# Kernel optimization log

Measured on AMD Instinct MI355X. Metric: run time of the kernel, lower is better.

Reference implementation:

```python
import jax, jax.numpy as jnp
import numpy as np

H = 16        # num heads
ALPHA = 1.3   # entmax alpha
N_ITER = 50   # bisection iterations
EPS = 1e-5    # layernorm eps


def entmax_bisect(x, alpha=ALPHA, n_iter=N_ITER):
    # x: (..., K). Bisection entmax along last axis (Peters et al. 2019).
    am1 = alpha - 1.0
    x = x - jnp.max(x, axis=-1, keepdims=True)
    m = jnp.max(x, axis=-1, keepdims=True)  # == 0 after shift
    lo, hi = m - 10.0, m + 10.0
    def step(carry, _):
        lo, hi = carry
        mid = 0.5 * (lo + hi)
        p = jnp.maximum(am1 * x - mid, 0.0) ** (1.0 / am1)
        gt = jnp.sum(p, axis=-1, keepdims=True) > 1.0
        return (jnp.where(gt, mid, lo), jnp.where(gt, hi, mid)), None
    (lo, hi), _ = jax.lax.scan(jax.checkpoint(step), (lo, hi), None, length=n_iter)
    p = jnp.maximum(am1 * x - hi, 0.0) ** (1.0 / am1)
    return p / (jnp.sum(p, axis=-1, keepdims=True) + 1e-12)


def _heads(t, B, N, hd):
    return t.reshape(B, N, H, hd).transpose(0, 2, 1, 3)  # (B,H,N,hd)


def attn_branch(x, mask, wq, bq, wk, bk, wv, bv, wo, bo, use_entmax):
    B, N, D = x.shape
    hd = D // H
    q = _heads(x @ wq + bq, B, N, hd)
    k = _heads(x @ wk + bk, B, N, hd)
    v = _heads(x @ wv + bv, B, N, hd)
    s = jnp.einsum('bhqd,bhkd->bhqk', q, k) / float(np.sqrt(hd)) + mask
    if use_entmax:
        s = s - jnp.max(s, axis=-1, keepdims=True)
        a = entmax_bisect(s)
    else:
        a = jax.nn.softmax(s, axis=-1)
    o = jnp.einsum('bhqk,bhkd->bhqd', a, v).transpose(0, 2, 1, 3).reshape(B, N, D)
    return o @ wo + bo


def layer_norm(x, g, b):
    m = jnp.mean(x, axis=-1, keepdims=True)
    v = jnp.mean((x - m) ** 2, axis=-1, keepdims=True)
    return (x - m) * jax.lax.rsqrt(v + EPS) * g + b


def setup_inputs():
    B, N, D, F, FILM, NMODS = 4, 512, 2048, 8192, 64, 10000
    key = jax.random.key(0)
    ks = iter(jax.random.split(key, 64))
    rn = lambda *s: jax.random.normal(next(ks), s, dtype=jnp.float32)
    inp = dict(
        x=rn(B, N, D),
        attn_mask_intra=jnp.zeros((N, N), jnp.float32),
        attn_mask_inter=jnp.zeros((N, N), jnp.float32),
        mods=jax.random.randint(next(ks), (B, N), 0, 9999),
        film_emb=rn(NMODS, FILM) * 0.02,
        film_gw=rn(FILM, D) * 0.02, film_gb=jnp.zeros((D,), jnp.float32),
        film_bw=rn(FILM, D) * 0.02, film_bb=jnp.zeros((D,), jnp.float32),
        gate_alpha=jnp.zeros((2,), jnp.float32),
        ln1_g=jnp.ones((D,), jnp.float32), ln1_b=jnp.zeros((D,), jnp.float32),
        ln2_g=jnp.ones((D,), jnp.float32), ln2_b=jnp.zeros((D,), jnp.float32),
        ffn_w1=rn(D, F) * 0.02, ffn_b1=jnp.zeros((F,), jnp.float32),
        ffn_w2=rn(F, D) * 0.02, ffn_b2=jnp.zeros((D,), jnp.float32),
    )
    for tag in ('a', 'e'):
        for nm in ('q', 'k', 'v', 'o'):
            inp['w%s_%s' % (nm, tag)] = rn(D, D) * 0.02
            inp['b%s_%s' % (nm, tag)] = jnp.zeros((D,), jnp.float32)
    return inp


def reference(x, attn_mask_intra, attn_mask_inter, mods,
              film_emb, film_gw, film_gb, film_bw, film_bb,
              gate_alpha, ln1_g, ln1_b, ln2_g, ln2_b,
              ffn_w1, ffn_b1, ffn_w2, ffn_b2,
              wq_a, bq_a, wk_a, bk_a, wv_a, bv_a, wo_a, bo_a,
              wq_e, bq_e, wk_e, bk_e, wv_e, bv_e, wo_e, bo_e):
    # FiLM modulation on the intra-module branch input
    e = film_emb[jnp.clip(mods, 1, None)]                      # (B,N,FILM)
    y_intra = (1.0 + e @ film_gw + film_gb) * x + (e @ film_bw + film_bb)
    z_intra = attn_branch(y_intra, attn_mask_intra, wq_a, bq_a, wk_a, bk_a,
                          wv_a, bv_a, wo_a, bo_a, use_entmax=False)
    z_inter = attn_branch(x, attn_mask_inter, wq_e, bq_e, wk_e, bk_e,
                          wv_e, bv_e, wo_e, bo_e, use_entmax=True)
    w = jax.nn.softmax(gate_alpha)                              # global gate
    z = w[0] * z_intra + w[1] * z_inter
    h = layer_norm(x + z, ln1_g, ln1_b)                         # Post-LN
    y = jax.nn.relu(h @ ffn_w1 + ffn_b1) @ ffn_w2 + ffn_b2
    return layer_norm(h + y, ln2_g, ln2_b)
```

## Files before the change

### kernel.cpp

```cpp
#include <hip/hip_runtime.h>
#include <hip/hip_bf16.h>

typedef float f32x4 __attribute__((ext_vector_type(4)));
typedef short bf16x8 __attribute__((ext_vector_type(8)));
typedef unsigned short u16;

#define SEQ    512
#define DIM    2048
#define NHEAD  16
#define HDIM   128
#define BATCH  4
#define BTOK   2048
#define FFDIM  8192
#define DSZ    ((long)BTOK*DIM)
#define QKVN   (3*DIM)
#define QKVSZ  ((long)BTOK*QKVN)
#define ISS    0.08838834764831845f

__device__ __forceinline__ u16 f2bf(float f){
  union{float fv;unsigned u;}c;c.fv=f;
  unsigned r=c.u+0x7FFFu+((c.u>>16)&1u); return (u16)(r>>16);
}
__device__ __forceinline__ float bf2f(u16 v){
  union{unsigned u;float f;}c;c.u=((unsigned)v)<<16;return c.f;
}
__device__ __forceinline__ float pow103(float t){
  return __builtin_amdgcn_exp2f(__builtin_amdgcn_logf(t)*(10.0f/3.0f));
}

#define GLD16(g,l) __builtin_amdgcn_global_load_lds( \
    (const __attribute__((address_space(1))) unsigned int*)(g), \
    (__attribute__((address_space(3))) unsigned int*)(l), 16, 0, 0)

#define MF(a,b,c) __builtin_amdgcn_mfma_f32_16x16x32_bf16(a,b,c,0,0,0)
#define VMW(n) do{ asm volatile("s_waitcnt vmcnt(" #n ")" ::: "memory"); \
                   __builtin_amdgcn_sched_barrier(0); }while(0)
#define LGKM0() do{ asm volatile("s_waitcnt lgkmcnt(0)" ::: "memory"); \
                    __builtin_amdgcn_sched_barrier(0); }while(0)
#define BARR() do{ asm volatile("" ::: "memory"); __builtin_amdgcn_s_barrier(); \
                   asm volatile("" ::: "memory"); }while(0)

__global__ __launch_bounds__(256, 2)
void gemm4w(const u16* __restrict__ A, int lda, long sAo, long sAi,
            const u16* __restrict__ B, int ldb, long sBo, long sBi,
            u16* __restrict__ C, int ldc, long sCo,
            const float* __restrict__ bias, long sbias,
            int K, int hdiv, int relu)
{
  __shared__ __align__(16) u16 sm[36864];
  char* smb = (char*)sm;

  int gx = gridDim.x, gy = gridDim.y;
  int nwg = gx*gy*gridDim.z;
  int flat = (blockIdx.z*gy + blockIdx.y)*gx + blockIdx.x;
  int cpx = nwg >> 3; flat = (flat & 7)*cpx + (flat >> 3);
  int by = flat % gy; int tq = flat / gy; int bx = tq % gx; int bz = tq / gx;

  int zo = bz / hdiv, zi = bz - zo*hdiv;
  const u16* Ab = A + (long)zo*sAo + (long)zi*sAi;
  const u16* Bb = B + (long)zo*sBo + (long)zi*sBi;
  int m0 = by*128, n0 = bx*256;

  int tid = threadIdx.x, lane = tid & 63, w = tid >> 6;
  int lr = lane & 15, lg = lane >> 4;
  int rl = lane >> 2, cbyte = (lane & 3)*16;

  int sRA[2], sCA[2];
  #pragma unroll
  for (int q = 0; q < 2; q++) {
    int r = (2*w+q)*16 + rl;
    sRA[q] = r ^ ((r>>2)&1);
    sCA[q] = (cbyte ^ ((((r>>2)^r)&1)<<4) ^ (((r>>1)&1)<<5)) >> 1;
  }
  int sRB[4], sCB[4];
  #pragma unroll
  for (int q = 0; q < 4; q++) {
    int r = (4*w+q)*16 + rl;
    sRB[q] = r ^ ((r>>2)&1);
    sCB[q] = (cbyte ^ ((((r>>2)^r)&1)<<4) ^ (((r>>1)&1)<<5)) >> 1;
  }

  int aoff = (lr*64 + lg*16) ^ ((lane&7)<<4);
  int boff = w*4096 + ((lr*64 + lg*16) ^ ((lane&7)<<4));

  f32x4 acc[8][4] = {};
  int NT = K >> 5;

  auto STG = [&](int buf, int kt) {
    int kcol = kt*32;
    char* base = smb + buf*24576;
    #pragma unroll
    for (int q = 0; q < 2; q++)
      GLD16(Ab + (long)(m0 + sRA[q])*lda + kcol + sCA[q], base + (2*w+q)*1024);
    #pragma unroll
    for (int q = 0; q < 4; q++)
      GLD16(Bb + (long)(n0 + sRB[q])*ldb + kcol + sCB[q], base + 8192 + (4*w+q)*1024);
  };

  STG(0,0);
  if (NT > 1) STG(1,1);

  int buf = 0;
  for (int t = 0; t < NT; t++) {
    char* Ax = smb + buf*24576;
    char* Bx = Ax + 8192;

    if (t+2 < NT) {
      int nb = buf + 2; if (nb >= 3) nb -= 3;
      STG(nb, t+2);
      VMW(12);
    } else if (t+1 < NT) { VMW(6); }
    else                 { VMW(0); }
    BARR();

    bf16x8 af[8], bv[4];
    #pragma unroll
    for (int i = 0; i < 8; i++) af[i] = *(const bf16x8*)(Ax + aoff + i*1024);
    #pragma unroll
    for (int j = 0; j < 4; j++) bv[j] = *(const bf16x8*)(Bx + boff + j*1024);
    LGKM0();
    __builtin_amdgcn_s_setprio(1);
    #pragma unroll
    for (int i = 0; i < 8; i++) {
      acc[i][0] = MF(af[i], bv[0], acc[i][0]);
      acc[i][1] = MF(af[i], bv[1], acc[i][1]);
      acc[i][2] = MF(af[i], bv[2], acc[i][2]);
      acc[i][3] = MF(af[i], bv[3], acc[i][3]);
    }
    __builtin_amdgcn_s_setprio(0);
    BARR();
    buf++; if (buf == 3) buf = 0;
  }

  u16* Cb = C + (long)bz*sCo;
  #pragma unroll
  for (int j = 0; j < 4; j++) {
    int col = n0 + w*64 + j*16 + lr;
    float bv2 = bias ? bias[zo*sbias + col] : 0.0f;
    #pragma unroll
    for (int i = 0; i < 8; i++) {
      #pragma unroll
      for (int e = 0; e < 4; e++) {
        int row = m0 + i*16 + lg*4 + e;
        float v = acc[i][j][e] + bv2;
        if (relu) v = fmaxf(v, 0.0f);
        Cb[(long)row*ldc + col] = f2bf(v);
      }
    }
  }
}

__global__ __launch_bounds__(256, 3)
void gemm4(const u16* __restrict__ A, int lda, long sAo, long sAi,
           const u16* __restrict__ B, int ldb, long sBo, long sBi,
           void* __restrict__ C, int ldc, long sCo, int outbf,
           const float* __restrict__ bias, long sbias,
           int K, int hdiv, int relu)
{
  __shared__ __align__(16) u16 sm[24576];
  char* smb = (char*)sm;

  int gx = gridDim.x, gy = gridDim.y;
  int nwg = gx*gy*gridDim.z;
  int flat = (blockIdx.z*gy + blockIdx.y)*gx + blockIdx.x;
  int cpx = nwg >> 3; flat = (flat & 7)*cpx + (flat >> 3);
  int by = flat % gy; int tq = flat / gy; int bx = tq % gx; int bz = tq / gx;

  int zo = bz / hdiv, zi = bz - zo*hdiv;
  const u16* Ab = A + (long)zo*sAo + (long)zi*sAi;
  const u16* Bb = B + (long)zo*sBo + (long)zi*sBi;
  int m0 = by*128, n0 = bx*128;

  int tid = threadIdx.x, lane = tid & 63, w = tid >> 6;
  int wrow = (w>>1)*64, wn = (w&1)*64;
  int lr = lane & 15, lg = lane >> 4;

  int stR[2], stC[2], ldsch[2];
  #pragma unroll
  for (int q = 0; q < 2; q++) {
    int chunk = q*4 + w;
    int r = chunk*16 + (lane>>2);
    int c = (lane&3)*16;
    int Rz = r ^ ((r>>2)&1);
    int Cz = c ^ ((((r>>2)^r)&1)<<4) ^ (((r>>1)&1)<<5);
    stR[q] = Rz; stC[q] = Cz>>1;
    ldsch[q] = chunk*1024;
  }

  int aoff = ((wrow + lr)*64 + lg*16) ^ ((lane&7)<<4);
  int boff = ((wn  + lr)*64 + lg*16) ^ ((lane&7)<<4);

  f32x4 acc[4][4] = {};
  int NT = K >> 5;

  auto STG = [&](int buf, int op, int kt) {
    const u16* gp = op ? Bb : Ab;
    int ld   = op ? ldb : lda;
    int base = op ? n0 : m0;
    int kcol = kt*32;
    #pragma unroll
    for (int q = 0; q < 2; q++) {
      const u16* src = gp + (long)(base + stR[q])*ld + kcol + stC[q];
      char* dst = smb + buf*16384 + op*8192 + ldsch[q];
      GLD16(src, dst);
    }
  };

  STG(0,0,0); STG(0,1,0);
  STG(1,0,1); STG(1,1,1);

  int buf = 0;
  for (int t = 0; t < NT; t++) {
    char* Ax = smb + buf*16384;
    char* Bx = smb + buf*16384 + 8192;

    if (t+2 < NT) {
      int nb = buf + 2; if (nb >= 3) nb -= 3;
      STG(nb,0,t+2); STG(nb,1,t+2);
      VMW(8);
    } else if (t+1 < NT) { VMW(4); }
    else                 { VMW(0); }
    BARR();

    bf16x8 af[4], bv[4];
    #pragma unroll
    for (int i = 0; i < 4; i++) af[i] = *(const bf16x8*)(Ax + aoff + i*1024);
    #pragma unroll
    for (int j = 0; j < 4; j++) bv[j] = *(const bf16x8*)(Bx + boff + j*1024);
    LGKM0();
    __builtin_amdgcn_s_setprio(1);
    #pragma unroll
    for (int i = 0; i < 4; i++) {
      acc[i][0] = MF(af[i], bv[0], acc[i][0]);
      acc[i][1] = MF(af[i], bv[1], acc[i][1]);
      acc[i][2] = MF(af[i], bv[2], acc[i][2]);
      acc[i][3] = MF(af[i], bv[3], acc[i][3]);
    }
    __builtin_amdgcn_s_setprio(0);
    BARR();
    buf++; if (buf == 3) buf = 0;
  }

  if (outbf) {
    u16* Cb = (u16*)C + (long)bz*sCo;
    #pragma unroll
    for (int j = 0; j < 4; j++) {
      int col = n0 + wn + j*16 + lr;
      float bv2 = bias ? bias[zo*sbias + col] : 0.0f;
      #pragma unroll
      for (int i = 0; i < 4; i++) {
        #pragma unroll
        for (int e = 0; e < 4; e++) {
          int row = m0 + wrow + i*16 + lg*4 + e;
          float v = acc[i][j][e] + bv2;
          if (relu) v = fmaxf(v, 0.0f);
          Cb[(long)row*ldc + col] = f2bf(v);
        }
      }
    }
  } else {
    float* Cb = (float*)C + (long)bz*sCo;
    #pragma unroll
    for (int j = 0; j < 4; j++) {
      int col = n0 + wn + j*16 + lr;
      #pragma unroll
      for (int i = 0; i < 4; i++) {
        #pragma unroll
        for (int e = 0; e < 4; e++) {
          int row = m0 + wrow + i*16 + lg*4 + e;
          Cb[(long)row*ldc + col] = acc[i][j][e];
        }
      }
    }
  }
}

template<int ENTMAX>
__global__ __launch_bounds__(256, 2)
void qkprobs(const u16* __restrict__ QKVp, long brOff,
             const float* __restrict__ maskp, u16* __restrict__ P)
{
  __shared__ __align__(16) u16 sm[40960];
  char* smb = (char*)sm;

  int m0 = blockIdx.x*64;
  int z  = blockIdx.y;
  int b  = z >> 4, h = z & 15;
  const u16* Qb = QKVp + brOff + (long)b*SEQ*QKVN + h*HDIM;
  const u16* Kb = Qb + DIM;

  int tid = threadIdx.x, lane = tid & 63, w = tid >> 6;
  int lr = lane & 15, lg = lane >> 4;
  int wn = w*128;

  int rl = lane >> 2;
  int cb = (lane & 3)*16;

  int aoff = (lr*64 + lg*16) ^ ((lane&7)<<4);
  int boff = ((wn + lr)*64 + lg*16) ^ ((lane&7)<<4);

  auto stgA = [&](int kt) {
    int r = w*16 + rl;
    int Rz = r ^ ((r>>2)&1);
    int Cz = cb ^ ((((r>>2)^r)&1)<<4) ^ (((r>>1)&1)<<5);
    GLD16(Qb + (long)(m0+Rz)*QKVN + kt*32 + (Cz>>1), smb + kt*4096 + w*1024);
  };
  auto stgB = [&](int buf, int kt) {
    #pragma unroll
    for (int q = 0; q < 8; q++) {
      int chunk = q*4 + w;
      int r = chunk*16 + rl;
      int Rz = r ^ ((r>>2)&1);
      int Cz = cb ^ ((((r>>2)^r)&1)<<4) ^ (((r>>1)&1)<<5);
      GLD16(Kb + (long)Rz*QKVN + kt*32 + (Cz>>1),
            smb + 16384 + buf*32768 + chunk*1024);
    }
  };

  f32x4 acc[4][8] = {};

  stgA(0); stgA(1); stgA(2); stgA(3);
  stgB(0,0);

  #pragma unroll
  for (int kt = 0; kt < 4; kt++) {
    if (kt < 3) { stgB((kt+1)&1, kt+1); VMW(8); } else { VMW(0); }
    BARR();
    char* Bx = smb + 16384 + (kt&1)*32768;
    bf16x8 af[4], bv[8];
    #pragma unroll
    for (int i = 0; i < 4; i++) af[i] = *(const bf16x8*)(smb + kt*4096 + aoff + i*1024);
    #pragma unroll
    for (int j = 0; j < 8; j++) bv[j] = *(const bf16x8*)(Bx + boff + j*1024);
    LGKM0();
    __builtin_amdgcn_s_setprio(1);
    #pragma unroll
    for (int i = 0; i < 4; i++)
      #pragma unroll
      for (int j = 0; j < 8; j++)
        acc[i][j] = MF(af[i], bv[j], acc[i][j]);
    __builtin_amdgcn_s_setprio(0);
    BARR();
  }

  float* redA = (float*)smb;
  float* redB = (float*)(smb + 1024);

  float rmax[16];
  #pragma unroll
  for (int s = 0; s < 16; s++) rmax[s] = -3.4e38f;
  #pragma unroll
  for (int i = 0; i < 4; i++) {
    #pragma unroll
    for (int e = 0; e < 4; e++) {
      int row = i*16 + lg*4 + e;
      const float* mp = maskp + (long)(m0+row)*SEQ + wn + lr;
      #pragma unroll
      for (int j = 0; j < 8; j++) {
        float v = acc[i][j][e]*ISS + mp[j*16];
        acc[i][j][e] = v;
        rmax[i*4+e] = fmaxf(rmax[i*4+e], v);
      }
    }
  }
  #pragma unroll
  for (int s = 0; s < 16; s++)
    #pragma unroll
    for (int o = 1; o < 16; o <<= 1) rmax[s] = fmaxf(rmax[s], __shfl_xor(rmax[s], o));
  if (lr == 0) {
    #pragma unroll
    for (int i = 0; i < 4; i++)
      #pragma unroll
      for (int e = 0; e < 4; e++) redA[w*64 + i*16 + lg*4 + e] = rmax[i*4+e];
  }
  BARR();
  #pragma unroll
  for (int i = 0; i < 4; i++)
    #pragma unroll
    for (int e = 0; e < 4; e++) {
      int row = i*16 + lg*4 + e;
      rmax[i*4+e] = fmaxf(fmaxf(redA[row], redA[64+row]),
                          fmaxf(redA[128+row], redA[192+row]));
    }
  BARR();

  float inv[16];

  if (ENTMAX) {
    #pragma unroll
    for (int i = 0; i < 4; i++)
      #pragma unroll
      for (int j = 0; j < 8; j++)
        #pragma unroll
        for (int e = 0; e < 4; e++)
          acc[i][j][e] = (acc[i][j][e] - rmax[i*4+e])*0.3f;

    float lo[16], hi[16], tau[16];
    #pragma unroll
    for (int s = 0; s < 16; s++) { lo[s] = -1.0f; hi[s] = 0.0f; }

    #pragma unroll 1
    for (int it = 0; it < 5; it++) {
      float ps[16];
      #pragma unroll
      for (int s = 0; s < 16; s++) ps[s] = 0.0f;
      #pragma unroll
      for (int i = 0; i < 4; i++)
        #pragma unroll
        for (int e = 0; e < 4; e++) {
          float mid = 0.5f*(lo[i*4+e] + hi[i*4+e]);
          #pragma unroll
          for (int j = 0; j < 8; j++) {
            float t = acc[i][j][e] - mid;
            if (t > 0.0f) ps[i*4+e] += pow103(t);
          }
        }
      #pragma unroll
      for (int s = 0; s < 16; s++)
        #pragma unroll
        for (int o = 1; o < 16; o <<= 1) ps[s] += __shfl_xor(ps[s], o);
      if (lr == 0) {
        #pragma unroll
        for (int i = 0; i < 4; i++)
          #pragma unroll
          for (int e = 0; e < 4; e++) redA[w*64 + i*16 + lg*4 + e] = ps[i*4+e];
      }
      BARR();
      #pragma unroll
      for (int i = 0; i < 4; i++)
        #pragma unroll
        for (int e = 0; e < 4; e++) {
          int row = i*16 + lg*4 + e, s = i*4+e;
          float tot = redA[row] + redA[64+row] + redA[128+row] + redA[192+row];
          float mid = 0.5f*(lo[s] + hi[s]);
          bool gt = tot > 1.0f;
          lo[s] = gt ? mid : lo[s];
          hi[s] = gt ? hi[s] : mid;
        }
      BARR();
    }
    #pragma unroll
    for (int s = 0; s < 16; s++) tau[s] = 0.5f*(lo[s] + hi[s]);

    #pragma unroll 1
    for (int it = 0; it < 5; it++) {
      float ps[16], pd[16];
      #pragma unroll
      for (int s = 0; s < 16; s++) { ps[s] = 0.0f; pd[s] = 0.0f; }
      #pragma unroll
      for (int i = 0; i < 4; i++)
        #pragma unroll
        for (int e = 0; e < 4; e++) {
          float tv = tau[i*4+e];
          #pragma unroll
          for (int j = 0; j < 8; j++) {
            float t = acc[i][j][e] - tv;
            if (t > 0.0f) {
              float w7 = __builtin_amdgcn_exp2f(__builtin_amdgcn_logf(t)*(7.0f/3.0f));
              pd[i*4+e] += w7; ps[i*4+e] += w7*t;
            }
          }
        }
      #pragma unroll
      for (int s = 0; s < 16; s++)
        #pragma unroll
        for (int o = 1; o < 16; o <<= 1) {
          ps[s] += __shfl_xor(ps[s], o);
          pd[s] += __shfl_xor(pd[s], o);
        }
      if (lr == 0) {
        #pragma unroll
        for (int i = 0; i < 4; i++)
          #pragma unroll
          for (int e = 0; e < 4; e++) {
            redA[w*64 + i*16 + lg*4 + e] = ps[i*4+e];
            redB[w*64 + i*16 + lg*4 + e] = pd[i*4+e];
          }
      }
      BARR();
      #pragma unroll
      for (int i = 0; i < 4; i++)
        #pragma unroll
        for (int e = 0; e < 4; e++) {
          int row = i*16 + lg*4 + e, s = i*4+e;
          float st = redA[row] + redA[64+row] + redA[128+row] + redA[192+row];
          float dt = redB[row] + redB[64+row] + redB[128+row] + redB[192+row];
          bool gt = st > 1.0f;
          lo[s] = gt ? tau[s] : lo[s];
          hi[s] = gt ? hi[s] : tau[s];
          float tn = tau[s] + (st - 1.0f) / ((10.0f/3.0f)*dt + 1e-30f);
          tau[s] = (tn > lo[s] && tn < hi[s]) ? tn : 0.5f*(lo[s] + hi[s]);
        }
      BARR();
    }

    float ps[16];
    #pragma unroll
    for (int s = 0; s < 16; s++) ps[s] = 0.0f;
    #pragma unroll
    for (int i = 0; i < 4; i++)
      #pragma unroll
      for (int e = 0; e < 4; e++) {
        float tv = tau[i*4+e];
        #pragma unroll
        for (int j = 0; j < 8; j++) {
          float t = acc[i][j][e] - tv;
          float p = (t > 0.0f) ? pow103(t) : 0.0f;
          acc[i][j][e] = p;
          ps[i*4+e] += p;
        }
      }
    #pragma unroll
    for (int s = 0; s < 16; s++)
      #pragma unroll
      for (int o = 1; o < 16; o <<= 1) ps[s] += __shfl_xor(ps[s], o);
    if (lr == 0) {
      #pragma unroll
      for (int i = 0; i < 4; i++)
        #pragma unroll
        for (int e = 0; e < 4; e++) redA[w*64 + i*16 + lg*4 + e] = ps[i*4+e];
    }
    BARR();
    #pragma unroll
    for (int i = 0; i < 4; i++)
      #pragma unroll
      for (int e = 0; e < 4; e++) {
        int row = i*16 + lg*4 + e;
        inv[i*4+e] = 1.0f/(redA[row] + redA[64+row] + redA[128+row] + redA[192+row] + 1e-12f);
      }
  } else {
    float ps[16];
    #pragma unroll
    for (int s = 0; s < 16; s++) ps[s] = 0.0f;
    #pragma unroll
    for (int i = 0; i < 4; i++)
      #pragma unroll
      for (int e = 0; e < 4; e++) {
        float mx = rmax[i*4+e];
        #pragma unroll
        for (int j = 0; j < 8; j++) {
          float p = __expf(acc[i][j][e] - mx);
          acc[i][j][e] = p;
          ps[i*4+e] += p;
        }
      }
    #pragma unroll
    for (int s = 0; s < 16; s++)
      #pragma unroll
      for (int o = 1; o < 16; o <<= 1) ps[s] += __shfl_xor(ps[s], o);
    if (lr == 0) {
      #pragma unroll
      for (int i = 0; i < 4; i++)
        #pragma unroll
        for (int e = 0; e < 4; e++) redA[w*64 + i*16 + lg*4 + e] = ps[i*4+e];
    }
    BARR();
    #pragma unroll
    for (int i = 0; i < 4; i++)
      #pragma unroll
      for (int e = 0; e < 4; e++) {
        int row = i*16 + lg*4 + e;
        inv[i*4+e] = 1.0f/(redA[row] + redA[64+row] + redA[128+row] + redA[192+row]);
      }
  }

  u16* Pb = P + ((long)z*SEQ + m0)*SEQ;
  #pragma unroll
  for (int i = 0; i < 4; i++)
    #pragma unroll
    for (int e = 0; e < 4; e++) {
      int row = i*16 + lg*4 + e;
      u16* pr = Pb + (long)row*SEQ + wn + lr;
      #pragma unroll
      for (int j = 0; j < 8; j++)
        pr[j*16] = f2bf(acc[i][j][e]*inv[i*4+e]);
    }
}

__global__ __launch_bounds__(256)
void redk(const float* __restrict__ Pp, int nk, const float* __restrict__ bias,
          u16* __restrict__ out)
{
  long i = ((long)blockIdx.x*256 + threadIdx.x)*8;
  long z = i >> 22;
  int  n = (int)(i & 2047);
  float v[8] = {};
  for (int k = 0; k < nk; k++) {
    const float* s = Pp + (z*nk + k)*DSZ + (i & (DSZ-1));
    f32x4 aa = *(const f32x4*)s, bb = *(const f32x4*)(s+4);
    v[0]+=aa.x; v[1]+=aa.y; v[2]+=aa.z; v[3]+=aa.w;
    v[4]+=bb.x; v[5]+=bb.y; v[6]+=bb.z; v[7]+=bb.w;
  }
  f32x4 b0 = *(const f32x4*)&bias[z*2048 + n], b1 = *(const f32x4*)&bias[z*2048 + n + 4];
  float bv[8] = {b0.x,b0.y,b0.z,b0.w,b1.x,b1.y,b1.z,b1.w};
  u16 w[8] __attribute__((aligned(16)));
  #pragma unroll
  for (int j = 0; j < 8; j++) w[j] = f2bf(v[j] + bv[j]);
  *(bf16x8*)&out[i] = *(bf16x8*)w;
}

template<int BN_, int WM_, int WN_>
__global__ __launch_bounds__(256)
void gemm_lds(const u16* __restrict__ A, int lda, long sAo, long sAi,
              const u16* __restrict__ B, int ldb, long sBo, long sBi,
              void* __restrict__ C, int ldc, long sCo, long sCi, int outbf,
              const float* __restrict__ bias, long sbias,
              float alpha, int K, int hdiv, int relu)
{
  constexpr int BM_ = 128;
  constexpr int MI = BM_/WM_/16;
  constexpr int NJ = BN_/WN_/16;
  __shared__ __align__(16) u16 As[BM_*32];
  __shared__ __align__(16) u16 Bs[BN_*32];

  int z = blockIdx.z, zo = z/hdiv, zi = z - zo*hdiv;
  const u16* Ab = A + zo*sAo + zi*sAi;
  const u16* Bb = B + zo*sBo + zi*sBi;

  int m0 = blockIdx.y*BM_, n0 = blockIdx.x*BN_;
  int tid = threadIdx.x, lane = tid & 63, wid = tid >> 6;
  int wrow = (wid/WN_)*(BM_/WM_), wcol = (wid%WN_)*(BN_/WN_);
  int lr = lane & 15, lg = lane >> 4;
  int srow = lane >> 2, skc = (lane & 3)*8;

  f32x4 acc[MI][NJ] = {};

  for (int k0 = 0; k0 < K; k0 += 32) {
    #pragma unroll
    for (int e = 0; e < BM_/64; e++) {
      int c = wid*(BM_/64) + e, row = c*16 + srow;
      GLD16(Ab + (long)(m0 + row)*lda + k0 + skc, &As[c*512]);
    }
    #pragma unroll
    for (int e = 0; e < BN_/64; e++) {
      int c = wid*(BN_/64) + e, row = c*16 + srow;
      GLD16(Bb + (long)(n0 + row)*ldb + k0 + skc, &Bs[c*512]);
    }
    __syncthreads();
    bf16x8 af[MI], bfv[NJ];
    #pragma unroll
    for (int i = 0; i < MI; i++)
      af[i] = *(const bf16x8*)&As[(wrow + i*16 + lr)*32 + lg*8];
    #pragma unroll
    for (int j = 0; j < NJ; j++)
      bfv[j] = *(const bf16x8*)&Bs[(wcol + j*16 + lr)*32 + lg*8];
    #pragma unroll
    for (int i = 0; i < MI; i++)
      #pragma unroll
      for (int j = 0; j < NJ; j++)
        acc[i][j] = MF(af[i], bfv[j], acc[i][j]);
    __syncthreads();
  }

  long coff = zo*sCo + zi*sCi;
  #pragma unroll
  for (int j = 0; j < NJ; j++) {
    int col = n0 + wcol + j*16 + lr;
    float bv = bias ? bias[zo*sbias + col] : 0.0f;
    #pragma unroll
    for (int i = 0; i < MI; i++) {
      #pragma unroll
      for (int e = 0; e < 4; e++) {
        int row = m0 + wrow + i*16 + lg*4 + e;
        float v = alpha*acc[i][j][e] + bv;
        if (relu)  v = fmaxf(v, 0.0f);
        long idx = coff + (long)row*ldc + col;
        if (outbf) ((u16*)C)[idx] = f2bf(v);
        else       ((float*)C)[idx] = v;
      }
    }
  }
}

struct P6 { const float* p[6]; };

__global__ __launch_bounds__(256)
void wtrans6(P6 srcs, int ldw, u16* __restrict__ Wt, long dstStride, int ldt)
{
  __shared__ u16 t[64][72];
  const float* W = srcs.p[blockIdx.z];
  u16* Wd = Wt + (long)blockIdx.z*dstStride;
  int tid = threadIdx.x, r = tid >> 2, c0 = (tid & 3)*16;
  long gr = (long)blockIdx.y*64 + r, gc = (long)blockIdx.x*64 + c0;
  #pragma unroll
  for (int u = 0; u < 16; u += 4) {
    f32x4 v = *(const f32x4*)&W[gr*ldw + gc + u];
    t[r][c0+u+0]=f2bf(v.x); t[r][c0+u+1]=f2bf(v.y);
    t[r][c0+u+2]=f2bf(v.z); t[r][c0+u+3]=f2bf(v.w);
  }
  __syncthreads();
  u16 o[16] __attribute__((aligned(16)));
  #pragma unroll
  for (int u = 0; u < 16; u++) o[u] = t[c0+u][r];
  u16* dst = &Wd[(long)(blockIdx.x*64 + r)*ldt + blockIdx.y*64 + c0];
  *(bf16x8*)&dst[0] = *(bf16x8*)&o[0];
  *(bf16x8*)&dst[8] = *(bf16x8*)&o[8];
}

__global__ __launch_bounds__(256)
void wtrans(const float* __restrict__ W, int ldw, u16* __restrict__ Wt, int ldt)
{
  __shared__ u16 t[64][72];
  int tid = threadIdx.x, r = tid >> 2, c0 = (tid & 3)*16;
  long gr = (long)blockIdx.y*64 + r, gc = (long)blockIdx.x*64 + c0;
  #pragma unroll
  for (int u = 0; u < 16; u += 4) {
    f32x4 v = *(const f32x4*)&W[gr*ldw + gc + u];
    t[r][c0+u+0]=f2bf(v.x); t[r][c0+u+1]=f2bf(v.y);
    t[r][c0+u+2]=f2bf(v.z); t[r][c0+u+3]=f2bf(v.w);
  }
  __syncthreads();
  u16 o[16] __attribute__((aligned(16)));
  #pragma unroll
  for (int u = 0; u < 16; u++) o[u] = t[c0+u][r];
  u16* dst = &Wt[(long)(blockIdx.x*64 + r)*ldt + blockIdx.y*64 + c0];
  *(bf16x8*)&dst[0] = *(bf16x8*)&o[0];
  *(bf16x8*)&dst[8] = *(bf16x8*)&o[8];
}

__global__ __launch_bounds__(256)
void vtrans(const u16* __restrict__ V, u16* __restrict__ Vt)
{
  __shared__ u16 t[64][72];
  int z = blockIdx.z, b = z >> 4, h = z & 15;
  const u16* src = V + (long)b*SEQ*QKVN + h*HDIM;
  u16* dst = Vt + (long)z*HDIM*SEQ;
  int tid = threadIdx.x, r = tid >> 2, c0 = (tid & 3)*16;
  int tok0 = blockIdx.x*64, d0 = blockIdx.y*64;
  #pragma unroll
  for (int u = 0; u < 16; u += 8) {
    bf16x8 v = *(const bf16x8*)&src[(long)(tok0+r)*QKVN + d0 + c0 + u];
    #pragma unroll
    for (int e = 0; e < 8; e++) t[r][c0+u+e] = (u16)v[e];
  }
  __syncthreads();
  u16 o[16] __attribute__((aligned(16)));
  #pragma unroll
  for (int u = 0; u < 16; u++) o[u] = t[c0+u][r];
  *(bf16x8*)&dst[(long)(d0+r)*SEQ + tok0 + c0]     = *(bf16x8*)&o[0];
  *(bf16x8*)&dst[(long)(d0+r)*SEQ + tok0 + c0 + 8] = *(bf16x8*)&o[8];
}

__global__ __launch_bounds__(256)
void f32_to_bf16(const float* __restrict__ in, u16* __restrict__ o, long n8)
{
  long i = (long)blockIdx.x*256 + threadIdx.x;
  if (i >= n8) return; i *= 8;
  f32x4 a = *(const f32x4*)&in[i], b = *(const f32x4*)&in[i+4];
  u16 w[8] __attribute__((aligned(16)));
  w[0]=f2bf(a.x);w[1]=f2bf(a.y);w[2]=f2bf(a.z);w[3]=f2bf(a.w);
  w[4]=f2bf(b.x);w[5]=f2bf(b.y);w[6]=f2bf(b.z);w[7]=f2bf(b.w);
  *(bf16x8*)&o[i] = *(bf16x8*)w;
}

__global__ __launch_bounds__(256)
void egather(const int* __restrict__ mods, const float* __restrict__ emb, u16* __restrict__ E)
{
  int i = blockIdx.x*256 + threadIdx.x;
  int row = i >> 3, j0 = (i & 7)*8;
  int m = mods[row]; if (m < 1) m = 1;
  const float* s = &emb[(long)m*64 + j0];
  f32x4 a = *(const f32x4*)s, b = *(const f32x4*)(s+4);
  u16 w[8] __attribute__((aligned(16)));
  w[0]=f2bf(a.x);w[1]=f2bf(a.y);w[2]=f2bf(a.z);w[3]=f2bf(a.w);
  w[4]=f2bf(b.x);w[5]=f2bf(b.y);w[6]=f2bf(b.z);w[7]=f2bf(b.w);
  *(bf16x8*)&E[(long)row*64 + j0] = *(bf16x8*)w;
}

__global__ __launch_bounds__(256)
void film_apply(const float* __restrict__ x, const u16* __restrict__ G,
                const u16* __restrict__ B, u16* __restrict__ y)
{
  long i = ((long)blockIdx.x*256 + threadIdx.x)*8;
  f32x4 x0 = *(const f32x4*)&x[i], x1 = *(const f32x4*)&x[i+4];
  bf16x8 g = *(const bf16x8*)&G[i], b = *(const bf16x8*)&B[i];
  float xv[8] = {x0.x,x0.y,x0.z,x0.w,x1.x,x1.y,x1.z,x1.w};
  u16 w[8] __attribute__((aligned(16)));
  #pragma unroll
  for (int e = 0; e < 8; e++)
    w[e] = f2bf((1.0f + bf2f((u16)g[e]))*xv[e] + bf2f((u16)b[e]));
  *(bf16x8*)&y[i] = *(bf16x8*)w;
}

__global__ __launch_bounds__(256)
void pack_bias(float* __restrict__ dst,
               const float* q_a, const float* k_a, const float* v_a,
               const float* q_e, const float* k_e, const float* v_e,
               const float* o_a, const float* o_e,
               const float* fg, const float* fb)
{
  int i = blockIdx.x*256 + threadIdx.x;
  if (i < 12288) {
    int br = i/6144, r = i - br*6144, sel = r >> 11, o = r & 2047;
    const float* s = br ? (sel==0?q_e:sel==1?k_e:v_e)
                        : (sel==0?q_a:sel==1?k_a:v_a);
    dst[i] = s[o];
  } else if (i < 16384) {
    int r = i - 12288; dst[i] = (r>>11) ? o_e[r&2047] : o_a[r&2047];
  } else {
    int r = i - 16384; dst[i] = (r>>11) ? fb[r&2047] : fg[r&2047];
  }
}

__global__ __launch_bounds__(256)
void ln_gate(const float* __restrict__ x, const u16* __restrict__ z0,
             const u16* __restrict__ z1, const float* __restrict__ ga,
             const float* __restrict__ g, const float* __restrict__ b,
             u16* __restrict__ h)
{
  __shared__ float red[8];
  long base = (long)blockIdx.x*DIM;
  int t8 = threadIdx.x*8, lane = threadIdx.x & 63, wid = threadIdx.x >> 6;
  float a0 = ga[0], a1 = ga[1];
  float mm = fmaxf(a0,a1), e0 = __expf(a0-mm), e1 = __expf(a1-mm);
  float w0 = e0/(e0+e1), w1 = e1/(e0+e1);
  f32x4 x0 = *(const f32x4*)&x[base+t8], x1 = *(const f32x4*)&x[base+t8+4];
  bf16x8 zi = *(const bf16x8*)&z0[base+t8], ze = *(const bf16x8*)&z1[base+t8];
  float xv[8] = {x0.x,x0.y,x0.z,x0.w,x1.x,x1.y,x1.z,x1.w};
  float v[8]; float s = 0.0f;
  #pragma unroll
  for (int j = 0; j < 8; j++) {
    v[j] = xv[j] + w0*bf2f((u16)zi[j]) + w1*bf2f((u16)ze[j]);
    s += v[j];
  }
  for (int o = 32; o; o >>= 1) s += __shfl_xor(s, o);
  if (lane == 0) red[wid] = s;
  __syncthreads();
  float mean = (red[0]+red[1]+red[2]+red[3])*(1.0f/DIM);
  float q = 0.0f;
  #pragma unroll
  for (int j = 0; j < 8; j++) { float d = v[j]-mean; q += d*d; }
  for (int o = 32; o; o >>= 1) q += __shfl_xor(q, o);
  if (lane == 0) red[4+wid] = q;
  __syncthreads();
  float inv = rsqrtf((red[4]+red[5]+red[6]+red[7])*(1.0f/DIM) + 1e-5f);
  f32x4 g0 = *(const f32x4*)&g[t8], g1 = *(const f32x4*)&g[t8+4];
  f32x4 b0 = *(const f32x4*)&b[t8], b1 = *(const f32x4*)&b[t8+4];
  float gv[8] = {g0.x,g0.y,g0.z,g0.w,g1.x,g1.y,g1.z,g1.w};
  float bv[8] = {b0.x,b0.y,b0.z,b0.w,b1.x,b1.y,b1.z,b1.w};
  u16 w[8] __attribute__((aligned(16)));
  #pragma unroll
  for (int j = 0; j < 8; j++) w[j] = f2bf((v[j]-mean)*inv*gv[j] + bv[j]);
  *(bf16x8*)&h[base+t8] = *(bf16x8*)w;
}

__global__ __launch_bounds__(256)
void ln_res(const u16* __restrict__ hin, const u16* __restrict__ y,
            const float* __restrict__ g, const float* __restrict__ b,
            float* __restrict__ out)
{
  __shared__ float red[8];
  long base = (long)blockIdx.x*DIM;
  int t8 = threadIdx.x*8, lane = threadIdx.x & 63, wid = threadIdx.x >> 6;
  bf16x8 hv = *(const bf16x8*)&hin[base+t8], yv = *(const bf16x8*)&y[base+t8];
  float v[8]; float s = 0.0f;
  #pragma unroll
  for (int j = 0; j < 8; j++) { v[j] = bf2f((u16)hv[j]) + bf2f((u16)yv[j]); s += v[j]; }
  for (int o = 32; o; o >>= 1) s += __shfl_xor(s, o);
  if (lane == 0) red[wid] = s;
  __syncthreads();
  float mean = (red[0]+red[1]+red[2]+red[3])*(1.0f/DIM);
  float q = 0.0f;
  #pragma unroll
  for (int j = 0; j < 8; j++) { float d = v[j]-mean; q += d*d; }
  for (int o = 32; o; o >>= 1) q += __shfl_xor(q, o);
  if (lane == 0) red[4+wid] = q;
  __syncthreads();
  float inv = rsqrtf((red[4]+red[5]+red[6]+red[7])*(1.0f/DIM) + 1e-5f);
  f32x4 g0 = *(const f32x4*)&g[t8], g1 = *(const f32x4*)&g[t8+4];
  f32x4 b0 = *(const f32x4*)&b[t8], b1 = *(const f32x4*)&b[t8+4];
  float gv[8] = {g0.x,g0.y,g0.z,g0.w,g1.x,g1.y,g1.z,g1.w};
  float bv[8] = {b0.x,b0.y,b0.z,b0.w,b1.x,b1.y,b1.z,b1.w};
  f32x4 o0, o1;
  #pragma unroll
  for (int j = 0; j < 4; j++) o0[j] = (v[j]-mean)*inv*gv[j] + bv[j];
  #pragma unroll
  for (int j = 0; j < 4; j++) o1[j] = (v[4+j]-mean)*inv*gv[4+j] + bv[4+j];
  *(f32x4*)&out[base+t8] = o0;
  *(f32x4*)&out[base+t8+4] = o1;
}

static void G128(hipStream_t st, const u16* A,int lda,long sAo,long sAi,
                 const u16* B,int ldb,long sBo,long sBi,
                 void* C,int ldc,long sCo,long sCi,int outbf,
                 const float* bias,long sbias,
                 float alpha,int M,int N,int K,int batch,int hdiv,int relu)
{
  gemm_lds<128,2,2><<<dim3(N/128,M/128,batch),dim3(256),0,st>>>(
      A,lda,sAo,sAi,B,ldb,sBo,sBi,C,ldc,sCo,sCi,outbf,bias,sbias,alpha,K,hdiv,relu);
}
static void G64(hipStream_t st, const u16* A,int lda,long sAo,long sAi,
                const u16* B,int ldb,long sBo,long sBi,
                void* C,int ldc,long sCo,long sCi,int outbf,
                const float* bias,long sbias,
                float alpha,int M,int N,int K,int batch,int hdiv,int relu)
{
  gemm_lds<64,4,1><<<dim3(N/64,M/128,batch),dim3(256),0,st>>>(
      A,lda,sAo,sAi,B,ldb,sBo,sBi,C,ldc,sCo,sCi,outbf,bias,sbias,alpha,K,hdiv,relu);
}
static void G4(hipStream_t st, const u16* A,int lda,long sAo,long sAi,
               const u16* B,int ldb,long sBo,long sBi,
               void* C,int ldc,long sCo,int outbf,
               const float* bias,long sbias,int M,int N,int K,int batch,int hdiv,int relu)
{
  gemm4<<<dim3(N/128,M/128,batch),dim3(256),0,st>>>(
      A,lda,sAo,sAi,B,ldb,sBo,sBi,C,ldc,sCo,outbf,bias,sbias,K,hdiv,relu);
}
static void G4W(hipStream_t st, const u16* A,int lda,long sAo,long sAi,
                const u16* B,int ldb,long sBo,long sBi,
                u16* C,int ldc,long sCo,
                const float* bias,long sbias,int M,int N,int K,int batch,int hdiv,int relu)
{
  gemm4w<<<dim3(N/256,M/128,batch),dim3(256),0,st>>>(
      A,lda,sAo,sAi,B,ldb,sBo,sBi,C,ldc,sCo,bias,sbias,K,hdiv,relu);
}

extern "C" void kernel_launch(void* const* d_in, const int* in_sizes, int n_in,
                              void* d_out, int out_size, void* d_ws, size_t ws_size,
                              hipStream_t stream)
{
  const float* x          = (const float*)d_in[0];
  const float* mask_intra = (const float*)d_in[1];
  const float* mask_inter = (const float*)d_in[2];
  const int*   mods       = (const int*)  d_in[3];
  const float* film_emb   = (const float*)d_in[4];
  const float* film_gw    = (const float*)d_in[5];
  const float* film_gb    = (const float*)d_in[6];
  const float* film_bw    = (const float*)d_in[7];
  const float* film_bb    = (const float*)d_in[8];
  const float* gate_alpha = (const float*)d_in[9];
  const float* ln1_g = (const float*)d_in[10];
  const float* ln1_b = (const float*)d_in[11];
  const float* ln2_g = (const float*)d_in[12];
  const float* ln2_b = (const float*)d_in[13];
  const float* ffn_w1 = (const float*)d_in[14];
  const float* ffn_b1 = (const float*)d_in[15];
  const float* ffn_w2 = (const float*)d_in[16];
  const float* ffn_b2 = (const float*)d_in[17];
  const float* wq_a = (const float*)d_in[18]; const float* bq_a = (const float*)d_in[19];
  const float* wk_a = (const float*)d_in[20]; const float* bk_a = (const float*)d_in[21];
  const float* wv_a = (const float*)d_in[22]; const float* bv_a = (const float*)d_in[23];
  const float* wo_a = (const float*)d_in[24]; const float* bo_a = (const float*)d_in[25];
  const float* wq_e = (const float*)d_in[26]; const float* bq_e = (const float*)d_in[27];
  const float* wk_e = (const float*)d_in[28]; const float* bk_e = (const float*)d_in[29];
  const float* wv_e = (const float*)d_in[30]; const float* bv_e = (const float*)d_in[31];
  const float* wo_e = (const float*)d_in[32]; const float* bo_e = (const float*)d_in[33];

  char* ws = (char*)d_ws;
  u16*   ybf  = (u16*)(ws);
  u16*   xbf  = (u16*)(ws + (8L<<20));
  u16*   QKV  = (u16*)(ws + (16L<<20));
  u16*   Gf   = QKV;
  u16*   Bfm  = QKV + DSZ;
  u16*   zbuf = (u16*)(ws + (16L<<20));
  u16*   hbf  = (u16*)(ws + (32L<<20));
  u16*   Wst  = (u16*)(ws + (64L<<20));
  u16*   mid  = (u16*)(ws + (96L<<20));
  u16*   P    = (u16*)(ws + (128L<<20));
  float* Pf2  = (float*)(ws + (128L<<20));
  u16*   f2o  = (u16*)(ws);
  u16*   Vt   = (u16*)(ws + (160L<<20));
  u16*   Ebuf = (u16*)(ws + (160L<<20));
  u16*   Wfm  = (u16*)(ws + (161L<<20));
  u16*   AO   = (u16*)(ws + (168L<<20));
  float* bpk  = (float*)(ws + (184L<<20));

  f32_to_bf16<<<2048,256,0,stream>>>(x, xbf, DSZ/8);
  egather<<<64,256,0,stream>>>(mods, film_emb, Ebuf);
  {
    P6 pf; pf.p[0]=film_gw; pf.p[1]=film_bw;
    pf.p[2]=film_gw; pf.p[3]=film_gw; pf.p[4]=film_gw; pf.p[5]=film_gw;
    wtrans6<<<dim3(32,1,2),256,0,stream>>>(pf, DIM, Wfm, (long)DIM*64, 64);
  }
  pack_bias<<<80,256,0,stream>>>(bpk, bq_a,bk_a,bv_a, bq_e,bk_e,bv_e, bo_a,bo_e, film_gb,film_bb);

  G128(stream, Ebuf,64,0,0, Wfm,64,(long)DIM*64,0, Gf,DIM,DSZ,0,1,
       bpk+16384,2048, 1.0f, BTOK,DIM,64, 2,1,0);
  film_apply<<<2048,256,0,stream>>>(x, Gf, Bfm, ybf);

  {
    P6 pq; pq.p[0]=wq_a; pq.p[1]=wk_a; pq.p[2]=wv_a;
    pq.p[3]=wq_e; pq.p[4]=wk_e; pq.p[5]=wv_e;
    wtrans6<<<dim3(32,32,6),256,0,stream>>>(pq, DIM, Wst, (long)DIM*DIM, DIM);
  }
  G4W(stream, ybf,DIM,DSZ,0, Wst,DIM,(long)QKVN*DIM,0, QKV,QKVN,QKVSZ,
      bpk,QKVN, BTOK,QKVN,DIM, 2,1, 0);

  for (int br = 0; br < 2; br++) {
    long brOff = (long)br*QKVSZ;
    const u16* Vb = QKV + brOff + 2*DIM;
    if (br == 0)
      qkprobs<0><<<dim3(8,64),dim3(256),0,stream>>>(QKV, brOff, mask_intra, P);
    else
      qkprobs<1><<<dim3(8,64),dim3(256),0,stream>>>(QKV, brOff, mask_inter, P);
    vtrans<<<dim3(8,2,64),256,0,stream>>>(Vb, Vt);
    G64(stream, P,SEQ,(long)NHEAD*SEQ*SEQ,(long)SEQ*SEQ,
        Vt,SEQ,(long)NHEAD*HDIM*SEQ,(long)HDIM*SEQ,
        AO + (long)br*DSZ,DIM,(long)SEQ*DIM,HDIM,1, nullptr,0,
        1.0f, SEQ,HDIM,SEQ, BATCH*NHEAD,NHEAD,0);
  }

  {
    P6 po; po.p[0]=wo_a; po.p[1]=wo_e;
    po.p[2]=wo_a; po.p[3]=wo_a; po.p[4]=wo_a; po.p[5]=wo_a;
    wtrans6<<<dim3(32,32,2),256,0,stream>>>(po, DIM, Wst, (long)DIM*DIM, DIM);
  }
  G4(stream, AO,DIM,DSZ,0, Wst,DIM,(long)DIM*DIM,0, zbuf,DIM,DSZ,1,
     bpk+12288,DIM, BTOK,DIM,DIM, 2,1, 0);

  ln_gate<<<2048,256,0,stream>>>(x, zbuf, zbuf+DSZ, gate_alpha, ln1_g, ln1_b, hbf);

  wtrans<<<dim3(128,32),256,0,stream>>>(ffn_w1, FFDIM, Wst, DIM);
  G4W(stream, hbf,DIM,0,0, Wst,DIM,0,0, mid,FFDIM,0,
      ffn_b1,0, BTOK,FFDIM,DIM, 1,1, 1);
  wtrans<<<dim3(32,128),256,0,stream>>>(ffn_w2, DIM, Wst, FFDIM);
  G4(stream, mid,FFDIM,4096,0, Wst,FFDIM,4096,0, Pf2,DIM,DSZ,0,
     nullptr,0, BTOK,DIM,4096, 2,1, 0);
  redk<<<2048,256,0,stream>>>(Pf2, 2, ffn_b2, f2o);

  ln_res<<<2048,256,0,stream>>>(hbf, f2o, ln2_g, ln2_b, (float*)d_out);
}
```

Measured before the change: 623.9 us.

## Merge both attention branches into single launches and use gemm4 for PV

```diff
diff --git a/kernel.cpp b/kernel.cpp
--- a/kernel.cpp
+++ b/kernel.cpp
@@ -153,7 +153,7 @@
 __global__ __launch_bounds__(256, 3)
 void gemm4(const u16* __restrict__ A, int lda, long sAo, long sAi,
            const u16* __restrict__ B, int ldb, long sBo, long sBi,
-           void* __restrict__ C, int ldc, long sCo, int outbf,
+           void* __restrict__ C, int ldc, long sCo, long sCi, int outbf,
            const float* __restrict__ bias, long sbias,
            int K, int hdiv, int relu)
 {
@@ -207,7 +207,7 @@
   };
 
   STG(0,0,0); STG(0,1,0);
-  STG(1,0,1); STG(1,1,1);
+  if (NT > 1) { STG(1,0,1); STG(1,1,1); }
 
   int buf = 0;
   for (int t = 0; t < NT; t++) {
@@ -241,8 +241,9 @@
     buf++; if (buf == 3) buf = 0;
   }
 
+  long coff = (long)zo*sCo + (long)zi*sCi;
   if (outbf) {
-    u16* Cb = (u16*)C + (long)bz*sCo;
+    u16* Cb = (u16*)C + coff;
     #pragma unroll
     for (int j = 0; j < 4; j++) {
       int col = n0 + wn + j*16 + lr;
@@ -259,7 +260,7 @@
       }
     }
   } else {
-    float* Cb = (float*)C + (long)bz*sCo;
+    float* Cb = (float*)C + coff;
     #pragma unroll
     for (int j = 0; j < 4; j++) {
       int col = n0 + wn + j*16 + lr;
@@ -275,19 +276,22 @@
   }
 }
 
-template<int ENTMAX>
 __global__ __launch_bounds__(256, 2)
-void qkprobs(const u16* __restrict__ QKVp, long brOff,
-             const float* __restrict__ maskp, u16* __restrict__ P)
+void qkprobs_both(const u16* __restrict__ QKVp,
+                  const float* __restrict__ maskI, const float* __restrict__ maskE,
+                  u16* __restrict__ Pall)
 {
   __shared__ __align__(16) u16 sm[40960];
   char* smb = (char*)sm;
 
   int m0 = blockIdx.x*64;
-  int z  = blockIdx.y;
+  int z2 = blockIdx.y;
+  int br = z2 >> 6, z = z2 & 63;
   int b  = z >> 4, h = z & 15;
-  const u16* Qb = QKVp + brOff + (long)b*SEQ*QKVN + h*HDIM;
+  const float* maskp = br ? maskE : maskI;
+  const u16* Qb = QKVp + (long)br*QKVSZ + (long)b*SEQ*QKVN + h*HDIM;
   const u16* Kb = Qb + DIM;
+  u16* P = Pall + (long)br*64*SEQ*SEQ;
 
   int tid = threadIdx.x, lane = tid & 63, w = tid >> 6;
   int lr = lane & 15, lg = lane >> 4;
@@ -386,7 +390,7 @@
 
   float inv[16];
 
-  if (ENTMAX) {
+  if (br) {
     #pragma unroll
     for (int i = 0; i < 4; i++)
       #pragma unroll
@@ -652,7 +656,7 @@
     __syncthreads();
   }
 
-  long coff = zo*sCo + zi*sCi;
+  long coff = (long)zo*sCo + (long)zi*sCi;
   #pragma unroll
   for (int j = 0; j < NJ; j++) {
     int col = n0 + wcol + j*16 + lr;
@@ -719,11 +723,12 @@
 }
 
 __global__ __launch_bounds__(256)
-void vtrans(const u16* __restrict__ V, u16* __restrict__ Vt)
+void vtrans_both(const u16* __restrict__ QKVp, u16* __restrict__ Vt)
 {
   __shared__ u16 t[64][72];
-  int z = blockIdx.z, b = z >> 4, h = z & 15;
-  const u16* src = V + (long)b*SEQ*QKVN + h*HDIM;
+  int z = blockIdx.z;
+  int br = z >> 6, zz = z & 63, b = zz >> 4, h = zz & 15;
+  const u16* src = QKVp + (long)br*QKVSZ + (long)b*SEQ*QKVN + h*HDIM + 2*DIM;
   u16* dst = Vt + (long)z*HDIM*SEQ;
   int tid = threadIdx.x, r = tid >> 2, c0 = (tid & 3)*16;
   int tok0 = blockIdx.x*64, d0 = blockIdx.y*64;
@@ -880,31 +885,13 @@
   *(f32x4*)&out[base+t8+4] = o1;
 }
 
-static void G128(hipStream_t st, const u16* A,int lda,long sAo,long sAi,
-                 const u16* B,int ldb,long sBo,long sBi,
-                 void* C,int ldc,long sCo,long sCi,int outbf,
-                 const float* bias,long sbias,
-                 float alpha,int M,int N,int K,int batch,int hdiv,int relu)
-{
-  gemm_lds<128,2,2><<<dim3(N/128,M/128,batch),dim3(256),0,st>>>(
-      A,lda,sAo,sAi,B,ldb,sBo,sBi,C,ldc,sCo,sCi,outbf,bias,sbias,alpha,K,hdiv,relu);
-}
-static void G64(hipStream_t st, const u16* A,int lda,long sAo,long sAi,
-                const u16* B,int ldb,long sBo,long sBi,
-                void* C,int ldc,long sCo,long sCi,int outbf,
-                const float* bias,long sbias,
-                float alpha,int M,int N,int K,int batch,int hdiv,int relu)
-{
-  gemm_lds<64,4,1><<<dim3(N/64,M/128,batch),dim3(256),0,st>>>(
-      A,lda,sAo,sAi,B,ldb,sBo,sBi,C,ldc,sCo,sCi,outbf,bias,sbias,alpha,K,hdiv,relu);
-}
 static void G4(hipStream_t st, const u16* A,int lda,long sAo,long sAi,
                const u16* B,int ldb,long sBo,long sBi,
-               void* C,int ldc,long sCo,int outbf,
+               void* C,int ldc,long sCo,long sCi,int outbf,
                const float* bias,long sbias,int M,int N,int K,int batch,int hdiv,int relu)
 {
   gemm4<<<dim3(N/128,M/128,batch),dim3(256),0,st>>>(
-      A,lda,sAo,sAi,B,ldb,sBo,sBi,C,ldc,sCo,outbf,bias,sbias,K,hdiv,relu);
+      A,lda,sAo,sAi,B,ldb,sBo,sBi,C,ldc,sCo,sCi,outbf,bias,sbias,K,hdiv,relu);
 }
 static void G4W(hipStream_t st, const u16* A,int lda,long sAo,long sAi,
                 const u16* B,int ldb,long sBo,long sBi,
@@ -949,21 +936,21 @@
   char* ws = (char*)d_ws;
   u16*   ybf  = (u16*)(ws);
   u16*   xbf  = (u16*)(ws + (8L<<20));
+  u16*   AO   = (u16*)(ws);
   u16*   QKV  = (u16*)(ws + (16L<<20));
   u16*   Gf   = QKV;
   u16*   Bfm  = QKV + DSZ;
   u16*   zbuf = (u16*)(ws + (16L<<20));
   u16*   hbf  = (u16*)(ws + (32L<<20));
   u16*   Wst  = (u16*)(ws + (64L<<20));
+  u16*   Pall = (u16*)(ws + (96L<<20));
   u16*   mid  = (u16*)(ws + (96L<<20));
-  u16*   P    = (u16*)(ws + (128L<<20));
   float* Pf2  = (float*)(ws + (128L<<20));
-  u16*   f2o  = (u16*)(ws);
+  u16*   f2o  = (u16*)(ws + (16L<<20));
   u16*   Vt   = (u16*)(ws + (160L<<20));
   u16*   Ebuf = (u16*)(ws + (160L<<20));
   u16*   Wfm  = (u16*)(ws + (161L<<20));
-  u16*   AO   = (u16*)(ws + (168L<<20));
-  float* bpk  = (float*)(ws + (184L<<20));
+  float* bpk  = (float*)(ws + (176L<<20));
 
   f32_to_bf16<<<2048,256,0,stream>>>(x, xbf, DSZ/8);
   egather<<<64,256,0,stream>>>(mods, film_emb, Ebuf);
@@ -974,8 +961,8 @@
   }
   pack_bias<<<80,256,0,stream>>>(bpk, bq_a,bk_a,bv_a, bq_e,bk_e,bv_e, bo_a,bo_e, film_gb,film_bb);
 
-  G128(stream, Ebuf,64,0,0, Wfm,64,(long)DIM*64,0, Gf,DIM,DSZ,0,1,
-       bpk+16384,2048, 1.0f, BTOK,DIM,64, 2,1,0);
+  G4(stream, Ebuf,64,0,0, Wfm,64,(long)DIM*64,0, Gf,DIM,DSZ,0,1,
+     bpk+16384,2048, BTOK,DIM,64, 2,1, 0);
   film_apply<<<2048,256,0,stream>>>(x, Gf, Bfm, ybf);
 
   {
@@ -986,26 +973,19 @@
   G4W(stream, ybf,DIM,DSZ,0, Wst,DIM,(long)QKVN*DIM,0, QKV,QKVN,QKVSZ,
       bpk,QKVN, BTOK,QKVN,DIM, 2,1, 0);
 
-  for (int br = 0; br < 2; br++) {
-    long brOff = (long)br*QKVSZ;
-    const u16* Vb = QKV + brOff + 2*DIM;
-    if (br == 0)
-      qkprobs<0><<<dim3(8,64),dim3(256),0,stream>>>(QKV, brOff, mask_intra, P);
-    else
-      qkprobs<1><<<dim3(8,64),dim3(256),0,stream>>>(QKV, brOff, mask_inter, P);
-    vtrans<<<dim3(8,2,64),256,0,stream>>>(Vb, Vt);
-    G64(stream, P,SEQ,(long)NHEAD*SEQ*SEQ,(long)SEQ*SEQ,
-        Vt,SEQ,(long)NHEAD*HDIM*SEQ,(long)HDIM*SEQ,
-        AO + (long)br*DSZ,DIM,(long)SEQ*DIM,HDIM,1, nullptr,0,
-        1.0f, SEQ,HDIM,SEQ, BATCH*NHEAD,NHEAD,0);
-  }
+  vtrans_both<<<dim3(8,2,128),256,0,stream>>>(QKV, Vt);
+  qkprobs_both<<<dim3(8,128),dim3(256),0,stream>>>(QKV, mask_intra, mask_inter, Pall);
+  G4(stream, Pall,SEQ,(long)16*SEQ*SEQ,(long)SEQ*SEQ,
+     Vt,SEQ,(long)16*HDIM*SEQ,(long)HDIM*SEQ,
+     AO,DIM,(long)SEQ*DIM,HDIM,1, nullptr,0,
+     SEQ,HDIM,SEQ, 128,16, 0);
 
   {
     P6 po; po.p[0]=wo_a; po.p[1]=wo_e;
     po.p[2]=wo_a; po.p[3]=wo_a; po.p[4]=wo_a; po.p[5]=wo_a;
     wtrans6<<<dim3(32,32,2),256,0,stream>>>(po, DIM, Wst, (long)DIM*DIM, DIM);
   }
-  G4(stream, AO,DIM,DSZ,0, Wst,DIM,(long)DIM*DIM,0, zbuf,DIM,DSZ,1,
+  G4(stream, AO,DIM,DSZ,0, Wst,DIM,(long)DIM*DIM,0, zbuf,DIM,DSZ,0,1,
      bpk+12288,DIM, BTOK,DIM,DIM, 2,1, 0);
 
   ln_gate<<<2048,256,0,stream>>>(x, zbuf, zbuf+DSZ, gate_alpha, ln1_g, ln1_b, hbf);
@@ -1014,7 +994,7 @@
   G4W(stream, hbf,DIM,0,0, Wst,DIM,0,0, mid,FFDIM,0,
       ffn_b1,0, BTOK,FFDIM,DIM, 1,1, 1);
   wtrans<<<dim3(32,128),256,0,stream>>>(ffn_w2, DIM, Wst, FFDIM);
-  G4(stream, mid,FFDIM,4096,0, Wst,FFDIM,4096,0, Pf2,DIM,DSZ,0,
+  G4(stream, mid,FFDIM,4096,0, Wst,FFDIM,4096,0, Pf2,DIM,DSZ,0,0,
      nullptr,0, BTOK,DIM,4096, 2,1, 0);
   redk<<<2048,256,0,stream>>>(Pf2, 2, ffn_b2, f2o);
 
```

Measured after the change: 621.7 us. Within noise of the previous version (-0.3%).
